# Kernel tuning notes

Measured on AMD Instinct MI355X. Metric: run time of the kernel, lower is better.

Reference implementation:

```python
import jax, jax.numpy as jnp
import numpy as np

B, C, F, W, H, E = 2, 8, 256, 512, 8, 4
HD = F // H

def mc_linear(x, w):
    # per-channel linear over features: (b,c,f,w) x (c,g,f) -> (b,c,g,w)
    return jnp.einsum('bcfw,cgf->bcgw', x, w)

def conv2d(x, k, b, ph, pw, groups=1):
    y = jax.lax.conv_general_dilated(x, k, (1, 1), ((ph, ph), (pw, pw)),
                                     dimension_numbers=('NCHW', 'OIHW', 'NCHW'),
                                     feature_group_count=groups)
    return y + b[None, :, None, None]

def mc_ln(x, g, b, eps=1e-5):
    # MultichannelLayerNorm: layernorm over features axis (dim 2), per-channel affine
    m = jnp.mean(x, axis=2, keepdims=True)
    v = jnp.var(x, axis=2, keepdims=True)
    return (x - m) * jax.lax.rsqrt(v + eps) * g[None, :, :, None] + b[None, :, :, None]

def sq_relu(x):
    return jnp.square(jax.nn.relu(x))

def rope(x):
    # x: (b,c,H,n,d); interleaved rotary (lucidrains rotary_embedding_torch)
    n, d = x.shape[-2], x.shape[-1]
    inv = 1.0 / (10000.0 ** (jnp.arange(0, d, 2, dtype=jnp.float32) / d))
    fr = jnp.arange(n, dtype=jnp.float32)[:, None] * inv[None, :]
    cos = jnp.repeat(jnp.cos(fr), 2, axis=-1)
    sin = jnp.repeat(jnp.sin(fr), 2, axis=-1)
    x2 = x.reshape(x.shape[:-1] + (d // 2, 2))
    xr = jnp.stack((-x2[..., 1], x2[..., 0]), axis=-1).reshape(x.shape)
    return x * cos + xr * sin

def mc_attn(x, mem, Wq, Kq, bq, Wk, Kk, bk, Wv, Kv, bv, Wo):
    b, c, f, w = x.shape
    def proj(t, Wl, Kc, bc):
        y = conv2d(mc_linear(t, Wl), Kc, bc, 0, 1)               # (b,c,f,w)
        y = y.transpose(0, 1, 3, 2).reshape(b, c, w, H, HD)
        return y.transpose(0, 1, 3, 2, 4)                        # (b,c,H,w,hd)
    q = rope(proj(x, Wq, Kq, bq))
    k = rope(proj(mem, Wk, Kk, bk))
    v = proj(mem, Wv, Kv, bv)
    # NOTE: original divides by sqrt(h) where h == features, not head_dim
    qk = jnp.einsum('bchnd,bchmd->bchnm', q, k) / jnp.sqrt(jnp.float32(f))
    a = jnp.einsum('bchnm,bchmd->bchnd', jax.nn.softmax(qk, axis=-1), v)
    a = a.transpose(0, 1, 3, 2, 4).reshape(b, c, w, f).transpose(0, 1, 3, 2)
    return mc_linear(a, Wo)

def _forward(x, skip, Wq, Kq, bq, Wk, Kk, bk, Wv, Kv, bv, Wo,
             norm_g, norm_b, c1a_w, c1a_b, c1b_w, c1b_b, c2_w, c2_b, w3, w4):
    att = lambda i, t, m: mc_attn(t, m, Wq[i], Kq[i], bq[i], Wk[i], Kk[i], bk[i],
                                  Wv[i], Kv[i], bv[i], Wo[i])
    h = x  # embed is Identity since channels == out_channels; dropout in eval mode
    z = mc_ln(h, norm_g[0], norm_b[0])
    h = h + att(0, z, z) + att(1, z, skip)
    z = mc_ln(h, norm_g[1], norm_b[1])
    za = sq_relu(conv2d(z, c1a_w, c1a_b, 5, 0, groups=C))   # FrameConv k=11 depthwise
    zb = conv2d(z, c1b_w, c1b_b, 3, 0, groups=C)            # FrameConv k=7 depthwise
    z = conv2d(mc_ln(za + zb, norm_g[2], norm_b[2]), c2_w, c2_b, 3, 0, groups=C)
    h = h + z
    z4 = mc_ln(h, norm_g[3], norm_b[3])
    h = h + att(2, z4, z4)
    h = h + att(3, mc_ln(h, norm_g[4], norm_b[4]), skip)
    z = mc_linear(sq_relu(mc_linear(mc_ln(h, norm_g[5], norm_b[5]), w3)), w4)
    h = h + z
    return jnp.concatenate((x, h), axis=1)

def setup_inputs():
    key = jax.random.key(0)
    ks = jax.random.split(key, 16)
    s = 0.02
    r = lambda k, shp: jax.random.normal(k, shp, dtype=jnp.float32) * s
    return dict(
        x=jax.random.normal(ks[0], (B, C, F, W), dtype=jnp.float32),
        skip=jax.random.normal(ks[1], (B, C, F, W), dtype=jnp.float32),
        Wq=r(ks[2], (4, C, F, F)), Kq=r(ks[3], (4, C, C, 1, 3)), bq=jnp.zeros((4, C), jnp.float32),
        Wk=r(ks[4], (4, C, F, F)), Kk=r(ks[5], (4, C, C, 1, 3)), bk=jnp.zeros((4, C), jnp.float32),
        Wv=r(ks[6], (4, C, F, F)), Kv=r(ks[7], (4, C, C, 1, 3)), bv=jnp.zeros((4, C), jnp.float32),
        Wo=r(ks[8], (4, C, F, F)),
        norm_g=jnp.ones((6, C, F), jnp.float32), norm_b=jnp.zeros((6, C, F), jnp.float32),
        c1a_w=r(ks[9], (C, 1, 11, 1)), c1a_b=jnp.zeros((C,), jnp.float32),
        c1b_w=r(ks[10], (C, 1, 7, 1)), c1b_b=jnp.zeros((C,), jnp.float32),
        c2_w=r(ks[11], (C, 1, 7, 1)), c2_b=jnp.zeros((C,), jnp.float32),
        w3=r(ks[12], (C, E, F)), w4=r(ks[13], (C, F, E)),
    )

def reference(x, skip, Wq, Kq, bq, Wk, Kk, bk, Wv, Kv, bv, Wo,
              norm_g, norm_b, c1a_w, c1a_b, c1b_w, c1b_b, c2_w, c2_b, w3, w4):
    return _forward(x, skip, Wq, Kq, bq, Wk, Kk, bk, Wv, Kv, bv, Wo,
                    norm_g, norm_b, c1a_w, c1a_b, c1b_w, c1b_b, c2_w, c2_b, w3, w4)
```

## Files before the change

kernel.cpp:

```cpp
#include <hip/hip_runtime.h>

#define B_ 2
#define C_ 8
#define F_ 256
#define W_ 512
#define H_ 8
#define FW_ (F_*W_)
#define CFW_ (C_*FW_)
#define OBS_ (2*CFW_)

typedef unsigned short u16;

__device__ __forceinline__ u16 f2bf(float f){
  unsigned u = __float_as_uint(f);
  u += 0x7fffu + ((u>>16)&1u);
  return (u16)(u>>16);
}
__device__ __forceinline__ float bf2f(u16 u){
  return __uint_as_float((unsigned)u<<16);
}

typedef __attribute__((ext_vector_type(8))) short bf16x8;
typedef __attribute__((ext_vector_type(4))) float f32x4;

__global__ __launch_bounds__(256)
void init_out(const float* __restrict__ x, float* __restrict__ out){
  int i = blockIdx.x*256 + threadIdx.x;
  int b = i >> 20;
  int r = i & (CFW_-1);
  float v = x[i];
  out[(size_t)b*OBS_ + r] = v;
  out[(size_t)b*OBS_ + CFW_ + r] = v;
}

__global__ void put_val(float* o, float v){ o[0] = v; }

__global__ __launch_bounds__(256)
void cvt4(const float* __restrict__ s0, const float* __restrict__ s1,
          const float* __restrict__ s2, const float* __restrict__ s3,
          u16* __restrict__ d0, u16* __restrict__ d1, u16* __restrict__ d2,
          u16* __restrict__ d3){
  int which = blockIdx.y;
  const float* s = which==0 ? s0 : which==1 ? s1 : which==2 ? s2 : s3;
  u16* d        = which==0 ? d0 : which==1 ? d1 : which==2 ? d2 : d3;
  int i = (blockIdx.x*256 + threadIdx.x)*4;
  float4 v = *(const float4*)(s + i);
  ushort4 o;
  o.x = f2bf(v.x); o.y = f2bf(v.y); o.z = f2bf(v.z); o.w = f2bf(v.w);
  *(ushort4*)(d + i) = o;
}

__global__ __launch_bounds__(256)
void cvtT(const float* __restrict__ src, u16* __restrict__ dst){
  __shared__ float Tin[64][65];
  int w0 = blockIdx.x*64, f0 = blockIdx.y*64;
  int bc = blockIdx.z; int b = bc >> 3, c = bc & 7;
  const float* s = src + (size_t)b*CFW_ + (size_t)c*FW_;
  int t = threadIdx.x;
  int r16 = t >> 4, c4 = (t & 15)*4;
  #pragma unroll
  for (int pass = 0; pass < 4; ++pass){
    int f = r16 + pass*16;
    float4 v = *(const float4*)(s + (size_t)(f0+f)*W_ + w0 + c4);
    Tin[f][c4+0] = v.x; Tin[f][c4+1] = v.y;
    Tin[f][c4+2] = v.z; Tin[f][c4+3] = v.w;
  }
  __syncthreads();
  u16* d = dst + (size_t)b*CFW_ + (size_t)c*FW_;
  #pragma unroll
  for (int pass = 0; pass < 4; ++pass){
    int w = r16 + pass*16;
    ushort4 o;
    o.x = f2bf(Tin[c4+0][w]); o.y = f2bf(Tin[c4+1][w]);
    o.z = f2bf(Tin[c4+2][w]); o.w = f2bf(Tin[c4+3][w]);
    *(ushort4*)(d + (size_t)(w0+w)*F_ + f0 + c4) = o;
  }
}

__global__ __launch_bounds__(256)
void ln32T(const float* __restrict__ X, long xbs, u16* __restrict__ Y, long ybs,
           const float* __restrict__ g, const float* __restrict__ bta){
  int wl = threadIdx.x & 31, fs = threadIdx.x >> 5;
  int w = blockIdx.x*32 + wl;
  int c = blockIdx.y;
  int b = blockIdx.z;
  const float* xb = X + (size_t)b*xbs + (size_t)c*FW_ + w;
  float v[32];
  float sum = 0.f, sq = 0.f;
  #pragma unroll
  for (int i = 0; i < 32; ++i){
    v[i] = xb[(size_t)(fs*32 + i)*W_];
    sum += v[i]; sq += v[i]*v[i];
  }
  __shared__ float Ss[8][32], Sq[8][32], Mu[32], Rs[32];
  Ss[fs][wl] = sum; Sq[fs][wl] = sq;
  __syncthreads();
  if (fs == 0){
    float s = 0.f, q = 0.f;
    #pragma unroll
    for (int j = 0; j < 8; ++j){ s += Ss[j][wl]; q += Sq[j][wl]; }
    float mu = s * (1.f/256.f);
    float var = q * (1.f/256.f) - mu*mu;
    Mu[wl] = mu; Rs[wl] = rsqrtf(var + 1e-5f);
  }
  __syncthreads();
  float mu = Mu[wl], rs = Rs[wl];
  u16* yb = Y + (size_t)b*ybs + ((size_t)c*W_ + w)*F_ + fs*32;
  #pragma unroll
  for (int i4 = 0; i4 < 8; ++i4){
    ushort4 o;
    int f = fs*32 + i4*4;
    o.x = f2bf((v[i4*4+0] - mu)*rs*g[c*F_ + f+0] + bta[c*F_ + f+0]);
    o.y = f2bf((v[i4*4+1] - mu)*rs*g[c*F_ + f+1] + bta[c*F_ + f+1]);
    o.z = f2bf((v[i4*4+2] - mu)*rs*g[c*F_ + f+2] + bta[c*F_ + f+2]);
    o.w = f2bf((v[i4*4+3] - mu)*rs*g[c*F_ + f+3] + bta[c*F_ + f+3]);
    *(ushort4*)(yb + i4*4) = o;
  }
}

__global__ __launch_bounds__(256)
void ln32f(const float* __restrict__ X, long xbs, float* __restrict__ Y, long ybs,
           const float* __restrict__ g, const float* __restrict__ bta){
  int wl = threadIdx.x & 31, fs = threadIdx.x >> 5;
  int w = blockIdx.x*32 + wl;
  int c = blockIdx.y;
  int b = blockIdx.z;
  const float* xb = X + (size_t)b*xbs + (size_t)c*FW_ + w;
  float v[32];
  float sum = 0.f, sq = 0.f;
  #pragma unroll
  for (int i = 0; i < 32; ++i){
    v[i] = xb[(size_t)(fs*32 + i)*W_];
    sum += v[i]; sq += v[i]*v[i];
  }
  __shared__ float Ss[8][32], Sq[8][32], Mu[32], Rs[32];
  Ss[fs][wl] = sum; Sq[fs][wl] = sq;
  __syncthreads();
  if (fs == 0){
    float s = 0.f, q = 0.f;
    #pragma unroll
    for (int j = 0; j < 8; ++j){ s += Ss[j][wl]; q += Sq[j][wl]; }
    float mu = s * (1.f/256.f);
    float var = q * (1.f/256.f) - mu*mu;
    Mu[wl] = mu; Rs[wl] = rsqrtf(var + 1e-5f);
  }
  __syncthreads();
  float mu = Mu[wl], rs = Rs[wl];
  float* yb = Y + (size_t)b*ybs + (size_t)c*FW_ + w;
  #pragma unroll
  for (int i = 0; i < 32; ++i){
    int f = fs*32 + i;
    yb[(size_t)f*W_] = (v[i] - mu)*rs*g[c*F_ + f] + bta[c*F_ + f];
  }
}

__global__ __launch_bounds__(256)
void gemm_qkv_b(const u16* __restrict__ wqb, const u16* __restrict__ wkb,
                const u16* __restrict__ wvb,
                const u16* __restrict__ srcq, const u16* __restrict__ srckv,
                u16* __restrict__ T){
  int zid = blockIdx.z;
  int proj = zid >> 4;
  int bc = zid & 15; int b = bc >> 3, c = bc & 7;
  const u16* src = (proj == 0) ? srcq : srckv;
  const u16* Wm  = (proj == 0) ? wqb : (proj == 1 ? wkb : wvb);
  const u16* AxT = src + (size_t)b*CFW_ + (size_t)c*FW_;
  const u16* Bw = Wm + (size_t)c*F_*F_;
  u16* Yb = T + (size_t)proj*2*CFW_ + (size_t)b*CFW_ + (size_t)c*FW_;

  int w0 = blockIdx.x * 64;
  int g0 = blockIdx.y * 64;
  int t = threadIdx.x, lane = t & 63, wv_ = t >> 6;
  int gq = lane >> 4, c16 = lane & 15;
  int wm = w0 + wv_*16 + c16;
  const f32x4 zero4 = {0.f,0.f,0.f,0.f};
  f32x4 acc[4] = {zero4, zero4, zero4, zero4};

  for (int k0 = 0; k0 < F_; k0 += 32){
    bf16x8 af = *(const bf16x8*)(AxT + (size_t)wm*F_ + k0 + 8*gq);
    #pragma unroll
    for (int nf = 0; nf < 4; ++nf){
      bf16x8 bfr = *(const bf16x8*)(Bw + (size_t)(g0 + nf*16 + c16)*F_ + k0 + 8*gq);
      acc[nf] = __builtin_amdgcn_mfma_f32_16x16x32_bf16(af, bfr, acc[nf], 0, 0, 0);
    }
  }
  int wout = w0 + wv_*16 + 4*gq;
  #pragma unroll
  for (int nf = 0; nf < 4; ++nf){
    ushort4 o;
    o.x = f2bf(acc[nf][0]); o.y = f2bf(acc[nf][1]);
    o.z = f2bf(acc[nf][2]); o.w = f2bf(acc[nf][3]);
    *(ushort4*)(Yb + (size_t)(g0 + nf*16 + c16)*W_ + wout) = o;
  }
}

__global__ __launch_bounds__(256)
void gemm_wo_b(const u16* __restrict__ wob, const u16* __restrict__ A,
               float* __restrict__ Y){
  int bc = blockIdx.z; int b = bc >> 3, c = bc & 7;
  const u16* AxT = A + (size_t)b*CFW_ + (size_t)c*FW_;
  const u16* Bw = wob + (size_t)c*F_*F_;
  float* Yb = Y + (size_t)b*OBS_ + (size_t)c*FW_;
  int w0 = blockIdx.x * 64;
  int g0 = blockIdx.y * 64;
  int t = threadIdx.x, lane = t & 63, wv_ = t >> 6;
  int gq = lane >> 4, c16 = lane & 15;
  int wm = w0 + wv_*16 + c16;
  const f32x4 zero4 = {0.f,0.f,0.f,0.f};
  f32x4 acc[4] = {zero4, zero4, zero4, zero4};

  for (int k0 = 0; k0 < F_; k0 += 32){
    bf16x8 af = *(const bf16x8*)(AxT + (size_t)wm*F_ + k0 + 8*gq);
    #pragma unroll
    for (int nf = 0; nf < 4; ++nf){
      bf16x8 bfr = *(const bf16x8*)(Bw + (size_t)(g0 + nf*16 + c16)*F_ + k0 + 8*gq);
      acc[nf] = __builtin_amdgcn_mfma_f32_16x16x32_bf16(af, bfr, acc[nf], 0, 0, 0);
    }
  }
  int wout = w0 + wv_*16 + 4*gq;
  #pragma unroll
  for (int nf = 0; nf < 4; ++nf){
    float* y = Yb + (size_t)(g0 + nf*16 + c16)*W_ + wout;
    float4 o = *(float4*)y;
    o.x += acc[nf][0]; o.y += acc[nf][1]; o.z += acc[nf][2]; o.w += acc[nf][3];
    *(float4*)y = o;
  }
}

__global__ __launch_bounds__(256)
void conv_rope_lds(const u16* __restrict__ T,
                   const float* __restrict__ Kq3, const float* __restrict__ bq,
                   const float* __restrict__ Kk3, const float* __restrict__ bk,
                   const float* __restrict__ Kv3, const float* __restrict__ bv,
                   u16* __restrict__ Q, u16* __restrict__ K,
                   u16* __restrict__ V){
  __shared__ float Tin[16][514];
  __shared__ float Kc[192];
  int bx = blockIdx.x;
  int jf = bx & 127;
  int b  = (bx >> 7) & 1;
  int p  = bx >> 8;
  const float* K3   = p==0 ? Kq3 : (p==1 ? Kk3 : Kv3);
  const float* bias = p==0 ? bq  : (p==1 ? bk  : bv);
  const u16* Tb = T + (size_t)p*2*CFW_ + (size_t)b*CFW_;
  u16* O = (p==0 ? Q : (p==1 ? K : V)) + (size_t)b*CFW_;
  int f0 = jf*2;
  int t = threadIdx.x;

  if (t < 192) Kc[t] = K3[t];
  if (t < 16){ Tin[t][0] = 0.f; Tin[t][513] = 0.f; }
  for (int li = t; li < 16*128; li += 256){
    int row = li >> 7;
    int c4  = li & 127;
    int ci = row >> 1, fsel = row & 1;
    ushort4 v4 = *(const ushort4*)(Tb + ((size_t)ci*F_ + f0 + fsel)*W_ + c4*4);
    float* dst = &Tin[row][1 + c4*4];
    dst[0] = bf2f(v4.x); dst[1] = bf2f(v4.y);
    dst[2] = bf2f(v4.z); dst[3] = bf2f(v4.w);
  }
  __syncthreads();

  int co = t >> 5;
  int wg = t & 31;
  int wbase = wg*16;
  float bs = bias[co];
  float a0[16], a1[16];
  #pragma unroll
  for (int i = 0; i < 16; ++i){ a0[i] = bs; a1[i] = bs; }
  #pragma unroll
  for (int ci = 0; ci < 8; ++ci){
    const float* r0 = &Tin[ci*2+0][1 + wbase];
    const float* r1 = &Tin[ci*2+1][1 + wbase];
    float k0 = Kc[(co*8+ci)*3+0], k1 = Kc[(co*8+ci)*3+1], k2 = Kc[(co*8+ci)*3+2];
    #pragma unroll
    for (int i = 0; i < 16; ++i){
      a0[i] += k0*r0[i-1] + k1*r0[i] + k2*r0[i+1];
      a1[i] += k0*r1[i-1] + k1*r1[i] + k2*r1[i+1];
    }
  }
  size_t obase = ((size_t)co*F_ + f0)*W_ + wbase;
  if (p < 2){
    int j = jf & 15;
    float inv = exp2f(-(float)j * 0.83048202372184f);
    float sv, cv, dsn, dcs;
    sincosf((float)wbase * inv, &sv, &cv);
    sincosf(inv, &dsn, &dcs);
    float scale = (p == 0) ? 0.0625f : 1.f;
    u16 o0[16], o1[16];
    #pragma unroll
    for (int i = 0; i < 16; ++i){
      o0[i] = f2bf((a0[i]*cv - a1[i]*sv)*scale);
      o1[i] = f2bf((a1[i]*cv + a0[i]*sv)*scale);
      float cn = cv*dcs - sv*dsn;
      sv = sv*dcs + cv*dsn;
      cv = cn;
    }
    #pragma unroll
    for (int q4 = 0; q4 < 4; ++q4){
      *(ushort4*)(O + obase + q4*4)      = make_ushort4(o0[q4*4],o0[q4*4+1],o0[q4*4+2],o0[q4*4+3]);
      *(ushort4*)(O + obase + W_ + q4*4) = make_ushort4(o1[q4*4],o1[q4*4+1],o1[q4*4+2],o1[q4*4+3]);
    }
  } else {
    #pragma unroll
    for (int q4 = 0; q4 < 4; ++q4){
      ushort4 p0, p1;
      p0.x = f2bf(a0[q4*4+0]); p0.y = f2bf(a0[q4*4+1]);
      p0.z = f2bf(a0[q4*4+2]); p0.w = f2bf(a0[q4*4+3]);
      p1.x = f2bf(a1[q4*4+0]); p1.y = f2bf(a1[q4*4+1]);
      p1.z = f2bf(a1[q4*4+2]); p1.w = f2bf(a1[q4*4+3]);
      *(ushort4*)(O + obase + q4*4)      = p0;
      *(ushort4*)(O + obase + W_ + q4*4) = p1;
    }
  }
}

__global__ __launch_bounds__(512)
void attn_mfma_b(const u16* __restrict__ q, const u16* __restrict__ k,
                 const u16* __restrict__ v, u16* __restrict__ aT){
  extern __shared__ __align__(16) unsigned char smem_dyn[];
  u16* ks = (u16*)smem_dyn;
  u16* vs = ks + 512*40;
  u16* ps = vs + 32*520;
  int bx = blockIdx.x;
  int b = bx >> 6;
  int ch = bx & 63;
  int h = ch & 7, c = ch >> 3;
  size_t base = (size_t)b*CFW_ + ((size_t)c*F_ + h*32)*W_;
  int t = threadIdx.x;
  int lane = t & 63, wv = t >> 6;
  int g = lane >> 4, c16 = lane & 15;

  int q0 = blockIdx.y*128 + wv*16;
  union { bf16x8 v8; u16 u[8]; } aq;
  #pragma unroll
  for (int j = 0; j < 8; ++j)
    aq.u[j] = q[base + (size_t)(8*g + j)*W_ + q0 + c16];

  for (int d = 0; d < 32; ++d)
    ks[t*40 + d] = k[base + (size_t)d*W_ + t];
  {
    int m8 = (t & 63)*8;
    #pragma unroll
    for (int it = 0; it < 4; ++it){
      int d = (t >> 6) + it*8;
      *(uint4*)(vs + (size_t)d*520 + m8) = *(const uint4*)(v + base + (size_t)d*W_ + m8);
    }
  }
  __syncthreads();

  u16* pw = ps + (size_t)wv*16*136;

  float mrun[4] = {-3e38f,-3e38f,-3e38f,-3e38f};
  float lrun[4] = {0.f,0.f,0.f,0.f};
  const f32x4 zero4 = {0.f,0.f,0.f,0.f};
  f32x4 outacc[2] = {zero4, zero4};

  for (int kt = 0; kt < 4; ++kt){
    f32x4 sv[8];
    #pragma unroll
    for (int mi = 0; mi < 8; ++mi){
      int m0 = kt*128 + mi*16;
      bf16x8 kb8 = *(const bf16x8*)(ks + (size_t)(m0 + c16)*40 + 8*g);
      sv[mi] = __builtin_amdgcn_mfma_f32_16x16x32_bf16(aq.v8, kb8, zero4, 0, 0, 0);
    }
    float pmax[4];
    #pragma unroll
    for (int r = 0; r < 4; ++r){
      float m = sv[0][r];
      #pragma unroll
      for (int mi = 1; mi < 8; ++mi) m = fmaxf(m, sv[mi][r]);
      pmax[r] = m;
    }
    #pragma unroll
    for (int mask = 1; mask <= 8; mask <<= 1){
      #pragma unroll
      for (int r = 0; r < 4; ++r)
        pmax[r] = fmaxf(pmax[r], __shfl_xor(pmax[r], mask));
    }
    float corr[4];
    #pragma unroll
    for (int r = 0; r < 4; ++r){
      float mn = fmaxf(mrun[r], pmax[r]);
      corr[r] = __expf(mrun[r] - mn);
      mrun[r] = mn;
      lrun[r] *= corr[r];
    }
    #pragma unroll
    for (int mi = 0; mi < 8; ++mi){
      #pragma unroll
      for (int r = 0; r < 4; ++r){
        float p = __expf(sv[mi][r] - mrun[r]);
        lrun[r] += p;
        pw[(size_t)(4*g + r)*136 + mi*16 + c16] = f2bf(p);
      }
    }
    f32x4 cv = {corr[0], corr[1], corr[2], corr[3]};
    outacc[0] *= cv;
    outacc[1] *= cv;
    #pragma unroll
    for (int mc = 0; mc < 4; ++mc){
      bf16x8 pa  = *(const bf16x8*)(pw + (size_t)c16*136 + mc*32 + 8*g);
      bf16x8 vb0 = *(const bf16x8*)(vs + (size_t)c16*520      + kt*128 + mc*32 + 8*g);
      bf16x8 vb1 = *(const bf16x8*)(vs + (size_t)(16+c16)*520 + kt*128 + mc*32 + 8*g);
      outacc[0] = __builtin_amdgcn_mfma_f32_16x16x32_bf16(pa, vb0, outacc[0], 0, 0, 0);
      outacc[1] = __builtin_amdgcn_mfma_f32_16x16x32_bf16(pa, vb1, outacc[1], 0, 0, 0);
    }
  }
  float L[4];
  #pragma unroll
  for (int r = 0; r < 4; ++r){
    float s = lrun[r];
    #pragma unroll
    for (int mask = 1; mask <= 8; mask <<= 1) s += __shfl_xor(s, mask);
    L[r] = s;
  }
  size_t tbase = (size_t)b*CFW_ + (size_t)c*FW_;
  #pragma unroll
  for (int dt = 0; dt < 2; ++dt){
    #pragma unroll
    for (int r = 0; r < 4; ++r)
      aT[tbase + (size_t)(q0 + 4*g + r)*F_ + h*32 + dt*16 + c16]
        = f2bf(outacc[dt][r] / L[r]);
  }
}

__global__ __launch_bounds__(256)
void dw_fuse_b(const float* __restrict__ Z, long zbs,
               const float* __restrict__ k11, const float* __restrict__ b11,
               const float* __restrict__ k7,  const float* __restrict__ b7,
               float* __restrict__ S, long sbs){
  int w = blockIdx.x*256 + threadIdx.x;
  int f = blockIdx.y;
  int bc = blockIdx.z; int b = bc >> 3, c = bc & 7;
  const float* zb = Z + (size_t)b*zbs + (size_t)c*FW_;
  float a = b11[c];
  #pragma unroll
  for (int i = 0; i < 11; ++i){
    int ff = f - 5 + i;
    if (ff >= 0 && ff < F_) a += k11[c*11 + i]*zb[(size_t)ff*W_ + w];
  }
  float bb = b7[c];
  #pragma unroll
  for (int i = 0; i < 7; ++i){
    int ff = f - 3 + i;
    if (ff >= 0 && ff < F_) bb += k7[c*7 + i]*zb[(size_t)ff*W_ + w];
  }
  float ra = a > 0.f ? a*a : 0.f;
  S[(size_t)b*sbs + ((size_t)c*F_ + f)*W_ + w] = ra + bb;
}

__global__ __launch_bounds__(256)
void conv7_add_b(const float* __restrict__ T, long tbs,
                 const float* __restrict__ k7, const float* __restrict__ b7,
                 float* __restrict__ Hp, long hbs){
  int w = blockIdx.x*256 + threadIdx.x;
  int f = blockIdx.y;
  int bc = blockIdx.z; int b = bc >> 3, c = bc & 7;
  const float* tb = T + (size_t)b*tbs + (size_t)c*FW_;
  float acc = b7[c];
  #pragma unroll
  for (int i = 0; i < 7; ++i){
    int ff = f - 3 + i;
    if (ff >= 0 && ff < F_) acc += k7[c*7 + i]*tb[(size_t)ff*W_ + w];
  }
  Hp[(size_t)b*hbs + ((size_t)c*F_ + f)*W_ + w] += acc;
}

__global__ __launch_bounds__(256)
void ff_ln(float* __restrict__ Hp,
           const float* __restrict__ g, const float* __restrict__ bta,
           const float* __restrict__ w3, const float* __restrict__ w4){
  int wl = threadIdx.x & 31, fs = threadIdx.x >> 5;
  int w = blockIdx.x*32 + wl;
  int c = blockIdx.y, b = blockIdx.z;
  float* hcol = Hp + (size_t)b*OBS_ + (size_t)c*FW_ + w;
  float v[32];
  float sum = 0.f, sq = 0.f;
  #pragma unroll
  for (int i = 0; i < 32; ++i){
    v[i] = hcol[(size_t)(fs*32 + i)*W_];
    sum += v[i]; sq += v[i]*v[i];
  }
  __shared__ float Ss[8][32], Sq[8][32], Mu[32], Rs[32];
  Ss[fs][wl] = sum; Sq[fs][wl] = sq;
  __syncthreads();
  if (fs == 0){
    float s = 0.f, q = 0.f;
    #pragma unroll
    for (int j = 0; j < 8; ++j){ s += Ss[j][wl]; q += Sq[j][wl]; }
    float mu = s * (1.f/256.f);
    Mu[wl] = mu; Rs[wl] = rsqrtf(q * (1.f/256.f) - mu*mu + 1e-5f);
  }
  __syncthreads();
  float mu = Mu[wl], rs = Rs[wl];
  float u[4] = {0.f,0.f,0.f,0.f};
  #pragma unroll
  for (int i = 0; i < 32; ++i){
    int f = fs*32 + i;
    float z = (v[i] - mu)*rs*g[c*F_ + f] + bta[c*F_ + f];
    #pragma unroll
    for (int e = 0; e < 4; ++e) u[e] += w3[(c*4 + e)*F_ + f]*z;
  }
  __shared__ float Us[8][4][32];
  #pragma unroll
  for (int e = 0; e < 4; ++e) Us[fs][e][wl] = u[e];
  __syncthreads();
  float uf[4];
  #pragma unroll
  for (int e = 0; e < 4; ++e){
    float s = 0.f;
    #pragma unroll
    for (int j = 0; j < 8; ++j) s += Us[j][e][wl];
    float rr = s > 0.f ? s : 0.f;
    uf[e] = rr*rr;
  }
  #pragma unroll
  for (int i = 0; i < 32; ++i){
    int f = fs*32 + i;
    const float* w4r = w4 + (c*F_ + f)*4;
    hcol[(size_t)f*W_] = v[i] + w4r[0]*uf[0] + w4r[1]*uf[1] + w4r[2]*uf[2] + w4r[3]*uf[3];
  }
}

extern "C" void kernel_launch(void* const* d_in, const int* in_sizes, int n_in,
                              void* d_out, int out_size, void* d_ws, size_t ws_size,
                              hipStream_t stream){
  const float* x    = (const float*)d_in[0];
  const float* skip = (const float*)d_in[1];
  const float* Wq   = (const float*)d_in[2];
  const float* Kq   = (const float*)d_in[3];
  const float* bq   = (const float*)d_in[4];
  const float* Wk   = (const float*)d_in[5];
  const float* Kk   = (const float*)d_in[6];
  const float* bk   = (const float*)d_in[7];
  const float* Wv   = (const float*)d_in[8];
  const float* Kv   = (const float*)d_in[9];
  const float* bv   = (const float*)d_in[10];
  const float* Wo   = (const float*)d_in[11];
  const float* ng   = (const float*)d_in[12];
  const float* nb   = (const float*)d_in[13];
  const float* c1aw = (const float*)d_in[14];
  const float* c1ab = (const float*)d_in[15];
  const float* c1bw = (const float*)d_in[16];
  const float* c1bb = (const float*)d_in[17];
  const float* c2w  = (const float*)d_in[18];
  const float* c2b  = (const float*)d_in[19];
  const float* w3   = (const float*)d_in[20];
  const float* w4   = (const float*)d_in[21];

  float* out = (float*)d_out;
  float* hp  = out + CFW_;

  char* wsb = (char*)d_ws;
  u16* WQb  = (u16*)(wsb);
  u16* WKb  = (u16*)(wsb + ((size_t)4  << 20));
  u16* WVb  = (u16*)(wsb + ((size_t)8  << 20));
  u16* WOb  = (u16*)(wsb + ((size_t)12 << 20));
  u16* skT  = (u16*)(wsb + ((size_t)16 << 20));
  u16* zT   = (u16*)(wsb + ((size_t)20 << 20));
  u16* tqkv = (u16*)(wsb + ((size_t)24 << 20));
  u16* qbB  = (u16*)(wsb + ((size_t)36 << 20));
  u16* kbB  = (u16*)(wsb + ((size_t)40 << 20));
  u16* vbB  = (u16*)(wsb + ((size_t)44 << 20));
  float* zf = (float*)(wsb + ((size_t)48 << 20));
  float* sf = (float*)(wsb + ((size_t)56 << 20));
  u16* aT   = tqkv;

  float code = 0.f;
  if (n_in != 22) code += 20000.f;
  if (out_size != 4194304) code += 80000.f;
  if (ws_size < ((size_t)64 << 20)) code += 160000.f;

  dim3 gGemmQKV(8, 4, 48);
  dim3 gGemmWo(8, 4, 16);
  dim3 gLn(16, 8, 2);
  dim3 gPix(2, F_, 16);
  dim3 gAttn(128, 4);
  dim3 gCvtT(8, 4, 16);
  const int attn_lds_bytes = (512*40 + 32*520 + 8*16*136) * 2;

  init_out<<<8192, 256, 0, stream>>>(x, out);
  cvt4<<<dim3(2048, 4), 256, 0, stream>>>(Wq, Wk, Wv, Wo, WQb, WKb, WVb, WOb);
  cvtT<<<gCvtT, 256, 0, stream>>>(skip, skT);

  auto do_attn = [&](int i, const u16* srcq, const u16* srckv){
    size_t wo16 = (size_t)i*C_*F_*F_;
    gemm_qkv_b<<<gGemmQKV, 256, 0, stream>>>(WQb + wo16, WKb + wo16, WVb + wo16,
                                             srcq, srckv, tqkv);
    conv_rope_lds<<<768, 256, 0, stream>>>(
        tqkv, Kq + i*C_*C_*3, bq + i*C_, Kk + i*C_*C_*3, bk + i*C_,
        Kv + i*C_*C_*3, bv + i*C_, qbB, kbB, vbB);
    attn_mfma_b<<<gAttn, 512, attn_lds_bytes, stream>>>(qbB, kbB, vbB, aT);
    gemm_wo_b<<<gGemmWo, 256, 0, stream>>>(WOb + wo16, aT, hp);
  };

  ln32T<<<gLn, 256, 0, stream>>>(x, CFW_, zT, CFW_, ng + 0*C_*F_, nb + 0*C_*F_);
  do_attn(0, zT, zT);
  do_attn(1, zT, skT);

  ln32f<<<gLn, 256, 0, stream>>>(hp, OBS_, zf, CFW_, ng + 1*C_*F_, nb + 1*C_*F_);
  dw_fuse_b<<<gPix, 256, 0, stream>>>(zf, CFW_, c1aw, c1ab, c1bw, c1bb, sf, CFW_);
  ln32f<<<gLn, 256, 0, stream>>>(sf, CFW_, zf, CFW_, ng + 2*C_*F_, nb + 2*C_*F_);
  conv7_add_b<<<gPix, 256, 0, stream>>>(zf, CFW_, c2w, c2b, hp, OBS_);

  ln32T<<<gLn, 256, 0, stream>>>(hp, OBS_, zT, CFW_, ng + 3*C_*F_, nb + 3*C_*F_);
  do_attn(2, zT, zT);

  ln32T<<<gLn, 256, 0, stream>>>(hp, OBS_, zT, CFW_, ng + 4*C_*F_, nb + 4*C_*F_);
  do_attn(3, zT, skT);

  ff_ln<<<gLn, 256, 0, stream>>>(hp, ng + 5*C_*F_, nb + 5*C_*F_, w3, w4);

  if (code != 0.f) put_val<<<1, 1, 0, stream>>>(out, code);
}
```

Baseline: 440.9 us.

## Batch the two independent first attention blocks into shared kernel launches

The first two attention blocks read the same normalized input and both accumulate into the same hidden buffer, so they are now run together. The QKV GEMM, conv+RoPE and attention kernels take a batch index and launch twice the grid. The Wo GEMM sums both blocks' projections inside one accumulator before a single read-modify-write of the output. This cuts kernel launches, gives the under-filled attention and conv grids more blocks to occupy the GPU, and halves the fp32 output traffic for those two blocks. In exchange the workspace requirement grows from 64 MB to 88 MB, and intermediate buffers were moved to new offsets.

After: 430.9 us. 2.3% less time.

```diff
diff --git a/kernel.cpp b/kernel.cpp
--- a/kernel.cpp
+++ b/kernel.cpp
@@ -155,18 +155,22 @@
 }
 
 __global__ __launch_bounds__(256)
-void gemm_qkv_b(const u16* __restrict__ wqb, const u16* __restrict__ wkb,
+void gemm_qkv_m(const u16* __restrict__ wqb, const u16* __restrict__ wkb,
                 const u16* __restrict__ wvb,
-                const u16* __restrict__ srcq, const u16* __restrict__ srckv,
-                u16* __restrict__ T){
+                const u16* __restrict__ srcq,
+                const u16* __restrict__ kv0, const u16* __restrict__ kv1,
+                u16* __restrict__ T, int i0, int i1){
   int zid = blockIdx.z;
-  int proj = zid >> 4;
-  int bc = zid & 15; int b = bc >> 3, c = bc & 7;
-  const u16* src = (proj == 0) ? srcq : srckv;
+  int att = (zid >= 48) ? 1 : 0;
+  int rest = zid - att*48;
+  int proj = rest >> 4;
+  int bc = rest & 15; int b = bc >> 3, c = bc & 7;
+  int wi = att ? i1 : i0;
+  const u16* src = (proj == 0) ? srcq : (att ? kv1 : kv0);
   const u16* Wm  = (proj == 0) ? wqb : (proj == 1 ? wkb : wvb);
   const u16* AxT = src + (size_t)b*CFW_ + (size_t)c*FW_;
-  const u16* Bw = Wm + (size_t)c*F_*F_;
-  u16* Yb = T + (size_t)proj*2*CFW_ + (size_t)b*CFW_ + (size_t)c*FW_;
+  const u16* Bw = Wm + (size_t)wi*C_*F_*F_ + (size_t)c*F_*F_;
+  u16* Yb = T + ((size_t)(att*3 + proj)*2 + b)*CFW_ + (size_t)c*FW_;
 
   int w0 = blockIdx.x * 64;
   int g0 = blockIdx.y * 64;
@@ -195,11 +199,9 @@
 }
 
 __global__ __launch_bounds__(256)
-void gemm_wo_b(const u16* __restrict__ wob, const u16* __restrict__ A,
-               float* __restrict__ Y){
+void gemm_wo_m(const u16* __restrict__ wob, const u16* __restrict__ A,
+               float* __restrict__ Y, int i0, int i1, int natt){
   int bc = blockIdx.z; int b = bc >> 3, c = bc & 7;
-  const u16* AxT = A + (size_t)b*CFW_ + (size_t)c*FW_;
-  const u16* Bw = wob + (size_t)c*F_*F_;
   float* Yb = Y + (size_t)b*OBS_ + (size_t)c*FW_;
   int w0 = blockIdx.x * 64;
   int g0 = blockIdx.y * 64;
@@ -209,12 +211,16 @@
   const f32x4 zero4 = {0.f,0.f,0.f,0.f};
   f32x4 acc[4] = {zero4, zero4, zero4, zero4};
 
-  for (int k0 = 0; k0 < F_; k0 += 32){
-    bf16x8 af = *(const bf16x8*)(AxT + (size_t)wm*F_ + k0 + 8*gq);
-    #pragma unroll
-    for (int nf = 0; nf < 4; ++nf){
-      bf16x8 bfr = *(const bf16x8*)(Bw + (size_t)(g0 + nf*16 + c16)*F_ + k0 + 8*gq);
-      acc[nf] = __builtin_amdgcn_mfma_f32_16x16x32_bf16(af, bfr, acc[nf], 0, 0, 0);
+  for (int att = 0; att < natt; ++att){
+    const u16* AxT = A + ((size_t)(att*2) + b)*CFW_ + (size_t)c*FW_;
+    const u16* Bw = wob + (size_t)(att ? i1 : i0)*C_*F_*F_ + (size_t)c*F_*F_;
+    for (int k0 = 0; k0 < F_; k0 += 32){
+      bf16x8 af = *(const bf16x8*)(AxT + (size_t)wm*F_ + k0 + 8*gq);
+      #pragma unroll
+      for (int nf = 0; nf < 4; ++nf){
+        bf16x8 bfr = *(const bf16x8*)(Bw + (size_t)(g0 + nf*16 + c16)*F_ + k0 + 8*gq);
+        acc[nf] = __builtin_amdgcn_mfma_f32_16x16x32_bf16(af, bfr, acc[nf], 0, 0, 0);
+      }
     }
   }
   int wout = w0 + wv_*16 + 4*gq;
@@ -228,22 +234,25 @@
 }
 
 __global__ __launch_bounds__(256)
-void conv_rope_lds(const u16* __restrict__ T,
-                   const float* __restrict__ Kq3, const float* __restrict__ bq,
-                   const float* __restrict__ Kk3, const float* __restrict__ bk,
-                   const float* __restrict__ Kv3, const float* __restrict__ bv,
-                   u16* __restrict__ Q, u16* __restrict__ K,
-                   u16* __restrict__ V){
+void conv_rope_m(const u16* __restrict__ T,
+                 const float* __restrict__ Kq3, const float* __restrict__ bq,
+                 const float* __restrict__ Kk3, const float* __restrict__ bk,
+                 const float* __restrict__ Kv3, const float* __restrict__ bv,
+                 u16* __restrict__ Q, u16* __restrict__ K,
+                 u16* __restrict__ V, int i0, int i1){
   __shared__ float Tin[16][514];
   __shared__ float Kc[192];
   int bx = blockIdx.x;
-  int jf = bx & 127;
-  int b  = (bx >> 7) & 1;
-  int p  = bx >> 8;
-  const float* K3   = p==0 ? Kq3 : (p==1 ? Kk3 : Kv3);
-  const float* bias = p==0 ? bq  : (p==1 ? bk  : bv);
-  const u16* Tb = T + (size_t)p*2*CFW_ + (size_t)b*CFW_;
-  u16* O = (p==0 ? Q : (p==1 ? K : V)) + (size_t)b*CFW_;
+  int att = (bx >= 768) ? 1 : 0;
+  int r = bx - att*768;
+  int jf = r & 127;
+  int b  = (r >> 7) & 1;
+  int p  = r >> 8;
+  int wi = att ? i1 : i0;
+  const float* K3   = (p==0 ? Kq3 : (p==1 ? Kk3 : Kv3)) + (size_t)wi*C_*C_*3;
+  const float* bias = (p==0 ? bq  : (p==1 ? bk  : bv)) + (size_t)wi*C_;
+  const u16* Tb = T + ((size_t)(att*3 + p)*2 + b)*CFW_;
+  u16* O = (p==0 ? Q : (p==1 ? K : V)) + ((size_t)att*2 + b)*CFW_;
   int f0 = jf*2;
   int t = threadIdx.x;
 
@@ -315,17 +324,20 @@
 }
 
 __global__ __launch_bounds__(512)
-void attn_mfma_b(const u16* __restrict__ q, const u16* __restrict__ k,
-                 const u16* __restrict__ v, u16* __restrict__ aT){
+void attn_m(const u16* __restrict__ q, const u16* __restrict__ k,
+            const u16* __restrict__ v, u16* __restrict__ aT){
   extern __shared__ __align__(16) unsigned char smem_dyn[];
   u16* ks = (u16*)smem_dyn;
   u16* vs = ks + 512*40;
   u16* ps = vs + 32*520;
   int bx = blockIdx.x;
-  int b = bx >> 6;
-  int ch = bx & 63;
+  int att = bx >> 7;
+  int rb = bx & 127;
+  int b = rb >> 6;
+  int ch = rb & 63;
   int h = ch & 7, c = ch >> 3;
-  size_t base = (size_t)b*CFW_ + ((size_t)c*F_ + h*32)*W_;
+  size_t slot = ((size_t)att*2 + b)*CFW_;
+  size_t base = slot + ((size_t)c*F_ + h*32)*W_;
   int t = threadIdx.x;
   int lane = t & 63, wv = t >> 6;
   int g = lane >> 4, c16 = lane & 15;
@@ -414,7 +426,7 @@
     for (int mask = 1; mask <= 8; mask <<= 1) s += __shfl_xor(s, mask);
     L[r] = s;
   }
-  size_t tbase = (size_t)b*CFW_ + (size_t)c*FW_;
+  size_t tbase = slot + (size_t)c*FW_;
   #pragma unroll
   for (int dt = 0; dt < 2; ++dt){
     #pragma unroll
@@ -559,23 +571,20 @@
   u16* skT  = (u16*)(wsb + ((size_t)16 << 20));
   u16* zT   = (u16*)(wsb + ((size_t)20 << 20));
   u16* tqkv = (u16*)(wsb + ((size_t)24 << 20));
-  u16* qbB  = (u16*)(wsb + ((size_t)36 << 20));
-  u16* kbB  = (u16*)(wsb + ((size_t)40 << 20));
-  u16* vbB  = (u16*)(wsb + ((size_t)44 << 20));
-  float* zf = (float*)(wsb + ((size_t)48 << 20));
-  float* sf = (float*)(wsb + ((size_t)56 << 20));
+  u16* qbB  = (u16*)(wsb + ((size_t)48 << 20));
+  u16* kbB  = (u16*)(wsb + ((size_t)56 << 20));
+  u16* vbB  = (u16*)(wsb + ((size_t)64 << 20));
+  float* zf = (float*)(wsb + ((size_t)72 << 20));
+  float* sf = (float*)(wsb + ((size_t)80 << 20));
   u16* aT   = tqkv;
 
   float code = 0.f;
   if (n_in != 22) code += 20000.f;
   if (out_size != 4194304) code += 80000.f;
-  if (ws_size < ((size_t)64 << 20)) code += 160000.f;
-
-  dim3 gGemmQKV(8, 4, 48);
-  dim3 gGemmWo(8, 4, 16);
+  if (ws_size < ((size_t)88 << 20)) code += 160000.f;
+
   dim3 gLn(16, 8, 2);
   dim3 gPix(2, F_, 16);
-  dim3 gAttn(128, 4);
   dim3 gCvtT(8, 4, 16);
   const int attn_lds_bytes = (512*40 + 32*520 + 8*16*136) * 2;
 
@@ -583,20 +592,17 @@
   cvt4<<<dim3(2048, 4), 256, 0, stream>>>(Wq, Wk, Wv, Wo, WQb, WKb, WVb, WOb);
   cvtT<<<gCvtT, 256, 0, stream>>>(skip, skT);
 
-  auto do_attn = [&](int i, const u16* srcq, const u16* srckv){
-    size_t wo16 = (size_t)i*C_*F_*F_;
-    gemm_qkv_b<<<gGemmQKV, 256, 0, stream>>>(WQb + wo16, WKb + wo16, WVb + wo16,
-                                             srcq, srckv, tqkv);
-    conv_rope_lds<<<768, 256, 0, stream>>>(
-        tqkv, Kq + i*C_*C_*3, bq + i*C_, Kk + i*C_*C_*3, bk + i*C_,
-        Kv + i*C_*C_*3, bv + i*C_, qbB, kbB, vbB);
-    attn_mfma_b<<<gAttn, 512, attn_lds_bytes, stream>>>(qbB, kbB, vbB, aT);
-    gemm_wo_b<<<gGemmWo, 256, 0, stream>>>(WOb + wo16, aT, hp);
+  auto do_attn = [&](int i0, const u16* kv0, int i1, const u16* kv1, int natt){
+    gemm_qkv_m<<<dim3(8, 4, 48*natt), 256, 0, stream>>>(
+        WQb, WKb, WVb, zT, kv0, kv1, tqkv, i0, i1);
+    conv_rope_m<<<768*natt, 256, 0, stream>>>(
+        tqkv, Kq, bq, Kk, bk, Kv, bv, qbB, kbB, vbB, i0, i1);
+    attn_m<<<dim3(128*natt, 4), 512, attn_lds_bytes, stream>>>(qbB, kbB, vbB, aT);
+    gemm_wo_m<<<dim3(8, 4, 16), 256, 0, stream>>>(WOb, aT, hp, i0, i1, natt);
   };
 
   ln32T<<<gLn, 256, 0, stream>>>(x, CFW_, zT, CFW_, ng + 0*C_*F_, nb + 0*C_*F_);
-  do_attn(0, zT, zT);
-  do_attn(1, zT, skT);
+  do_attn(0, zT, 1, skT, 2);
 
   ln32f<<<gLn, 256, 0, stream>>>(hp, OBS_, zf, CFW_, ng + 1*C_*F_, nb + 1*C_*F_);
   dw_fuse_b<<<gPix, 256, 0, stream>>>(zf, CFW_, c1aw, c1ab, c1bw, c1bb, sf, CFW_);
@@ -604,10 +610,10 @@
   conv7_add_b<<<gPix, 256, 0, stream>>>(zf, CFW_, c2w, c2b, hp, OBS_);
 
   ln32T<<<gLn, 256, 0, stream>>>(hp, OBS_, zT, CFW_, ng + 3*C_*F_, nb + 3*C_*F_);
-  do_attn(2, zT, zT);
+  do_attn(2, zT, 2, zT, 1);
 
   ln32T<<<gLn, 256, 0, stream>>>(hp, OBS_, zT, CFW_, ng + 4*C_*F_, nb + 4*C_*F_);
-  do_attn(3, zT, skT);
+  do_attn(3, skT, 3, skT, 1);
 
   ff_ln<<<gLn, 256, 0, stream>>>(hp, ng + 5*C_*F_, nb + 5*C_*F_, w3, w4);
 
```
